# Kernel tuning notes

Measured on AMD Instinct MI355X. Metric: run time of the kernel, lower is better.

Reference implementation:

```python
import jax, jax.numpy as jnp
import numpy as np

DT = 0.2
N_VAR = 6
FEAT = 32


def _constants():
    dt = DT
    H = np.zeros((2, N_VAR), np.float32); H[0, 0] = 1.0; H[1, 3] = 1.0
    F = np.eye(N_VAR, dtype=np.float32)
    F[0, 1] = dt; F[0, 2] = dt * dt / 2; F[1, 2] = dt
    F[3, 4] = dt; F[3, 5] = dt * dt / 2; F[4, 5] = dt
    G = np.zeros((N_VAR, 2), np.float32)
    G[0, 0] = dt ** 3 / 6; G[1, 0] = dt * dt / 2; G[2, 0] = dt
    G[3, 1] = dt ** 3 / 6; G[4, 1] = dt * dt / 2; G[5, 1] = dt
    Bm = G.copy()  # B matrix equals G_ numerically
    return jnp.asarray(H), jnp.asarray(F), jnp.asarray(G), jnp.asarray(Bm)


def _inv2x2(S):
    a = S[..., 0, 0]; b = S[..., 0, 1]; c = S[..., 1, 0]; d = S[..., 1, 1]
    det = a * d - b * c
    inv = jnp.stack([jnp.stack([d, -b], -1), jnp.stack([-c, a], -1)], -2)
    return inv / det[..., None, None]


def _lstm(x, h, c, Wih, Whh, bih, bhh):
    gates = x @ Wih.T + bih + h @ Whh.T + bhh
    i, f, g, o = jnp.split(gates, 4, axis=-1)
    c2 = jax.nn.sigmoid(f) * c + jax.nn.sigmoid(i) * jnp.tanh(g)
    h2 = jax.nn.sigmoid(o) * jnp.tanh(c2)
    return h2, c2


def _forward(hist, position_std_x, position_std_y, velocity_std_x, velocity_std_y,
             acceleration_std_x, acceleration_std_y, jerk_std, coef_G, GR,
             cf_W, cf_b, lstm_Wih, lstm_Whh, lstm_bih, lstm_bhh, co_W, co_b, len_pred):
    H, F, G, Bm = _constants()
    Bsz = hist.shape[1]
    Z = hist[..., None]                          # (T, B, 2, 1)
    tanhG = jnp.tanh(coef_G)                     # (6,1)
    R = GR[:, None] * GR[None, :]                # (2,2)
    Gs_hist = G * tanhG * jerk_std               # (6,2)
    Q_hist = Gs_hist @ Gs_hist.T                 # (6,6)
    Id = jnp.eye(N_VAR, dtype=hist.dtype)

    # Kalman init
    V0 = (Z[1] - Z[0]) / DT                      # (B,2,1)
    X = jnp.einsum('ij,bjk->bik', H.T, Z[0])     # (B,6,1)
    X = X.at[:, 1, 0].set(V0[:, 0, 0]).at[:, 3, 0].set(V0[:, 1, 0])
    diagv = jnp.concatenate([position_std_x ** 2, velocity_std_x ** 2, acceleration_std_x ** 2,
                             position_std_y ** 2, velocity_std_y ** 2, acceleration_std_y ** 2])
    P = jnp.broadcast_to(jnp.diag(diagv), (Bsz, N_VAR, N_VAR)).astype(hist.dtype)
    h = jnp.zeros((Bsz, FEAT), hist.dtype)
    c = jnp.zeros((Bsz, FEAT), hist.dtype)

    def hist_step(carry, Zt):
        X, P, h, c = carry
        # LSTM state update (command output is discarded during history filtering)
        feat = jnp.tanh(X[:, :, 0] @ cf_W.T + cf_b)
        h, c = _lstm(feat, h, c, lstm_Wih, lstm_Whh, lstm_bih, lstm_bhh)
        # predict (no command)
        X = jnp.einsum('ij,bjk->bik', F, X)
        P = jnp.einsum('ij,bjk,lk->bil', F, P, F) + Q_hist
        # innovation
        y = Zt - jnp.einsum('ij,bjk->bik', H, X)
        S = jnp.einsum('ij,bjk,lk->bil', H, P, H) + R
        # update
        Sinv = _inv2x2(S)
        K = jnp.einsum('bij,kj,bkl->bil', P, H, Sinv)          # (B,6,2)
        X = X + K @ y
        ImKH = Id - jnp.einsum('bij,jk->bik', K, H)
        P = jnp.einsum('bij,bjk,blk->bil', ImKH, P, ImKH) + jnp.einsum('bij,jk,blk->bil', K, R, K)
        return (X, P, h, c), None

    (X, P, h, c), _ = jax.lax.scan(hist_step, (X, P, h, c), Z[1:])

    GtG = G * tanhG                                            # (6,2)

    def pred_step(carry, _):
        X, P, h, c = carry
        feat = jnp.tanh(X[:, :, 0] @ cf_W.T + cf_b)
        h, c = _lstm(feat, h, c, lstm_Wih, lstm_Whh, lstm_bih, lstm_bhh)
        command = h @ co_W.T + co_b                            # (B,4)
        X = jnp.einsum('ij,bjk->bik', F, X) + jnp.einsum('ij,bj->bi', Bm, command[:, :2])[:, :, None]
        Gs = jnp.einsum('ij,bj->bi', GtG, command[:, 2:])      # (B,6)
        Q = jnp.einsum('bi,bj->bij', Gs, Gs)
        P = jnp.einsum('ij,bjk,lk->bil', F, P, F) + Q
        mu = jnp.einsum('ij,bjk->bik', H, X)[:, :, 0]          # (B,2)
        Pout = jnp.einsum('ij,bjk,lk->bil', H, P, H)           # (B,2,2)
        return (X, P, h, c), (mu, Pout)

    _, (mu, Pout) = jax.lax.scan(pred_step, (X, P, h, c), None, length=len_pred)
    sx = jnp.sqrt(Pout[:, :, 0, 0])[..., None]
    sy = jnp.sqrt(Pout[:, :, 1, 1])[..., None]
    rho = (Pout[:, :, 0, 1] + Pout[:, :, 1, 0])[..., None] / (2 * sx * sy)
    return jnp.concatenate([mu, sx, sy, rho], axis=2)          # (len_pred, B, 5)


def setup_inputs() -> dict:
    key = jax.random.key(0)
    ks = jax.random.split(key, 8)
    T, B = 16, 32768
    u = lambda k, shape, fan: jax.random.uniform(k, shape, jnp.float32, -1.0, 1.0) / np.sqrt(fan)
    return {
        'hist': jax.random.normal(ks[0], (T, B, 2), jnp.float32),
        'position_std_x': jnp.ones((1,), jnp.float32) * 0.0519,
        'position_std_y': jnp.ones((1,), jnp.float32) * 1.7321,
        'velocity_std_x': jnp.ones((1,), jnp.float32) * 0.036,
        'velocity_std_y': jnp.ones((1,), jnp.float32) * 19.8837,
        'acceleration_std_x': jnp.ones((1,), jnp.float32) * 1e-05,
        'acceleration_std_y': jnp.ones((1,), jnp.float32) * 5.34,
        'jerk_std': jnp.array([[3.5043, 17.0283]], jnp.float32),
        'coef_G': jnp.array([[0.7427], [2.3545], [-0.0247], [-0.1391], [9.011], [0.0963]], jnp.float32),
        'GR': jnp.array([-0.0015, 0.001], jnp.float32),
        'cf_W': u(ks[1], (FEAT, N_VAR), N_VAR),
        'cf_b': u(ks[2], (FEAT,), N_VAR),
        'lstm_Wih': u(ks[3], (4 * FEAT, FEAT), FEAT),
        'lstm_Whh': u(ks[4], (4 * FEAT, FEAT), FEAT),
        'lstm_bih': u(ks[5], (4 * FEAT,), FEAT),
        'lstm_bhh': u(ks[6], (4 * FEAT,), FEAT),
        'co_W': u(ks[7], (4, FEAT), FEAT),
        'co_b': jnp.zeros((4,), jnp.float32),
        'len_pred': 25,
    }


def reference(hist, position_std_x, position_std_y, velocity_std_x, velocity_std_y,
              acceleration_std_x, acceleration_std_y, jerk_std, coef_G, GR,
              cf_W, cf_b, lstm_Wih, lstm_Whh, lstm_bih, lstm_bhh, co_W, co_b, len_pred):
    return _forward(hist, position_std_x, position_std_y, velocity_std_x, velocity_std_y,
                    acceleration_std_x, acceleration_std_y, jerk_std, coef_G, GR,
                    cf_W, cf_b, lstm_Wih, lstm_Whh, lstm_bih, lstm_bhh, co_W, co_b, int(len_pred))
```

## Files before the change

### kernel.cpp

```cpp
#include <hip/hip_runtime.h>
#include <hip/hip_bf16.h>
#include <math.h>

#define BLK 64
#define EPB 16
#define NF 32
#define THIST 15

typedef __attribute__((ext_vector_type(8))) short s16x8;
typedef __attribute__((ext_vector_type(4))) float f32x4;
typedef __attribute__((ext_vector_type(2))) float f32x2;

union frag_u { s16x8 v; unsigned u[4]; };

__device__ __forceinline__ float frcp(float x) {
    return __builtin_amdgcn_rcpf(x);
}
__device__ __forceinline__ float exp2b(float x) {
    return __builtin_amdgcn_exp2f(x);
}
__device__ __forceinline__ unsigned packbf2(float x0, float x1) {
    __hip_bfloat162 b = __float22bfloat162_rn(float2{x0, x1});
    union { __hip_bfloat162 b; unsigned u; } c; c.b = b; return c.u;
}
__device__ __forceinline__ float tanhfe(float x) {
    float e = __expf(2.0f * x);
    return fmaf(-2.0f, frcp(e + 1.0f), 1.0f);
}

__device__ __forceinline__ void fpft(float (&P)[6][6]) {
    const float dt = 0.2f, hd = 0.02f;
    #pragma unroll
    for (int j = 0; j < 6; ++j) {
        float a0 = P[0][j] + dt * P[1][j] + hd * P[2][j];
        float a1 = P[1][j] + dt * P[2][j];
        float a3 = P[3][j] + dt * P[4][j] + hd * P[5][j];
        float a4 = P[4][j] + dt * P[5][j];
        P[0][j] = a0; P[1][j] = a1; P[3][j] = a3; P[4][j] = a4;
    }
    #pragma unroll
    for (int i = 0; i < 6; ++i) {
        float a0 = P[i][0] + dt * P[i][1] + hd * P[i][2];
        float a1 = P[i][1] + dt * P[i][2];
        float a3 = P[i][3] + dt * P[i][4] + hd * P[i][5];
        float a4 = P[i][4] + dt * P[i][5];
        P[i][0] = a0; P[i][1] = a1; P[i][3] = a3; P[i][4] = a4;
    }
}

__global__ __launch_bounds__(BLK, 2)
void kalman_lstm(const float* __restrict__ hist,
                 const float* __restrict__ psx, const float* __restrict__ psy,
                 const float* __restrict__ vsx, const float* __restrict__ vsy,
                 const float* __restrict__ asx, const float* __restrict__ asy,
                 const float* __restrict__ jerk, const float* __restrict__ coefG,
                 const float* __restrict__ GRv,
                 const float* __restrict__ cfW, const float* __restrict__ cfb,
                 const float* __restrict__ Wih, const float* __restrict__ Whh,
                 const float* __restrict__ bih, const float* __restrict__ bhh,
                 const float* __restrict__ coW, const float* __restrict__ cob,
                 float* __restrict__ out, int B, int len_pred)
{
    __shared__ float kf[216];

    const int lane = threadIdx.x;
    const int e = lane & 15;
    const int s = lane >> 4;
    const int b = blockIdx.x * EPB + e;

    const float dt = 0.2f, hd = 0.02f;
    const float g0 = dt * dt * dt / 6.0f, g1 = 0.02f, g2 = dt;
    const float NL2E  = -1.4426950408889634f;
    const float T2L2E =  2.8853900817779268f;
    float ga0 = g0 * tanhf(coefG[0]);
    float ga1 = g1 * tanhf(coefG[1]);
    float ga2 = g2 * tanhf(coefG[2]);
    float gb3 = g0 * tanhf(coefG[3]);
    float gb4 = g1 * tanhf(coefG[4]);
    float gb5 = g2 * tanhf(coefG[5]);

    {
        float j0 = jerk[0], j1 = jerk[1];
        float gr0 = GRv[0], gr1 = GRv[1];
        float R00 = gr0 * gr0, R01 = gr0 * gr1, R11 = gr1 * gr1;
        float qa[3] = {ga0 * j0, ga1 * j0, ga2 * j0};
        float qb[3] = {gb3 * j1, gb4 * j1, gb5 * j1};

        float Pk[6][6];
        #pragma unroll
        for (int i = 0; i < 6; ++i)
            #pragma unroll
            for (int j = 0; j < 6; ++j) Pk[i][j] = 0.0f;
        { float v;
          v = psx[0]; Pk[0][0] = v * v;
          v = vsx[0]; Pk[1][1] = v * v;
          v = asx[0]; Pk[2][2] = v * v;
          v = psy[0]; Pk[3][3] = v * v;
          v = vsy[0]; Pk[4][4] = v * v;
          v = asy[0]; Pk[5][5] = v * v; }

        #pragma unroll 1
        for (int t = 0; t < THIST; ++t) {
            fpft(Pk);
            #pragma unroll
            for (int i = 0; i < 3; ++i)
                #pragma unroll
                for (int j = 0; j < 3; ++j) {
                    Pk[i][j]         += qa[i] * qa[j];
                    Pk[3 + i][3 + j] += qb[i] * qb[j];
                }
            float S00 = Pk[0][0] + R00;
            float S01 = Pk[0][3] + R01;
            float S11 = Pk[3][3] + R11;
            float idet = 1.0f / (S00 * S11 - S01 * S01);
            float i00 =  S11 * idet, i01 = -S01 * idet, i11 = S00 * idet;
            float K0[6], K1[6];
            #pragma unroll
            for (int i = 0; i < 6; ++i) {
                K0[i] = Pk[i][0] * i00 + Pk[i][3] * i01;
                K1[i] = Pk[i][0] * i01 + Pk[i][3] * i11;
            }
            if (lane == 0) {
                #pragma unroll
                for (int i = 0; i < 3; ++i) {
                    kf[t * 12 + 2 * i]     = K0[i];
                    kf[t * 12 + 2 * i + 1] = K0[3 + i];
                    kf[t * 12 + 6 + 2 * i]     = K1[i];
                    kf[t * 12 + 6 + 2 * i + 1] = K1[3 + i];
                }
            }
            #pragma unroll
            for (int i = 0; i < 6; ++i) {
                Pk[i][1] -= K0[1] * Pk[i][0] + K1[1] * Pk[i][3];
                Pk[i][2] -= K0[2] * Pk[i][0] + K1[2] * Pk[i][3];
                Pk[i][4] -= K0[4] * Pk[i][0] + K1[4] * Pk[i][3];
                Pk[i][5] -= K0[5] * Pk[i][0] + K1[5] * Pk[i][3];
                float t0 = Pk[i][0] - (K0[0] * Pk[i][0] + K1[0] * Pk[i][3]);
                float t3 = Pk[i][3] - (K0[3] * Pk[i][0] + K1[3] * Pk[i][3]);
                Pk[i][0] = t0; Pk[i][3] = t3;
            }
        }
        if (lane == 0) {
            #pragma unroll
            for (int i = 0; i < 6; ++i)
                #pragma unroll
                for (int j = 0; j < 6; ++j) kf[180 + i * 6 + j] = Pk[i][j];
        }
    }

    s16x8 wih_h[8], whh_h[8];
    #pragma unroll
    for (int nt = 0; nt < 8; ++nt) {
        int G = nt >> 1, blk = nt & 1;
        float sc = (G == 2) ? T2L2E : NL2E;
        int base = (G * 32 + 8 * (e >> 2) + 4 * blk + (e & 3)) * NF + s * 8;
        frag_u ih_h, hh_h;
        #pragma unroll
        for (int q = 0; q < 4; ++q) {
            ih_h.u[q] = packbf2(sc * Wih[base + 2 * q], sc * Wih[base + 2 * q + 1]);
            hh_h.u[q] = packbf2(sc * Whh[base + 2 * q], sc * Whh[base + 2 * q + 1]);
        }
        wih_h[nt] = ih_h.v;
        whh_h[nt] = hh_h.v;
    }

    f32x4 biasF[8];
    #pragma unroll
    for (int nt = 0; nt < 8; ++nt) {
        int G = nt >> 1, blk = nt & 1;
        float sc = (G == 2) ? T2L2E : NL2E;
        int base = G * 32 + 8 * s + 4 * blk;
        f32x4 bi = *(const f32x4*)&bih[base];
        f32x4 bh = *(const f32x4*)&bhh[base];
        biasF[nt] = (bi + bh) * sc;
    }

    s16x8 cfwA0, cfwA1;
    {
        frag_u fa0, fa1; fa0.v = (s16x8)0; fa1.v = (s16x8)0;
        if (s == 0) {
            int f0 = 8 * (e >> 2) + (e & 3);
            int f1 = f0 + 4;
            const float* w0 = cfW + f0 * 6;
            const float* w1 = cfW + f1 * 6;
            fa0.u[0] = packbf2(T2L2E * w0[0], T2L2E * w0[1]);
            fa0.u[1] = packbf2(T2L2E * w0[2], T2L2E * w0[3]);
            fa0.u[2] = packbf2(T2L2E * w0[4], T2L2E * w0[5]);
            fa0.u[3] = packbf2(T2L2E * cfb[f0], 0.0f);
            fa1.u[0] = packbf2(T2L2E * w1[0], T2L2E * w1[1]);
            fa1.u[1] = packbf2(T2L2E * w1[2], T2L2E * w1[3]);
            fa1.u[2] = packbf2(T2L2E * w1[4], T2L2E * w1[5]);
            fa1.u[3] = packbf2(T2L2E * cfb[f1], 0.0f);
        }
        cfwA0 = fa0.v; cfwA1 = fa1.v;
    }
    s16x8 cmdA;
    {
        frag_u ca;
        const float* cp = coW + (e & 3) * NF + 8 * s;
        #pragma unroll
        for (int q = 0; q < 4; ++q)
            ca.u[q] = packbf2(cp[2 * q], cp[2 * q + 1]);
        cmdA = ca.v;
    }
    f32x4 cobC = {cob[0], cob[1], cob[2], cob[3]};

    const float2* hist2 = (const float2*)hist;
    float2 z0 = hist2[b];
    float2 z1 = hist2[B + b];
    f32x2 Xa = {z0.x, (z1.y - z0.y) / dt};
    f32x2 Xb = {(z1.x - z0.x) / dt, 0.0f};
    f32x2 Xc = {0.0f, 0.0f};

    f32x2 creg2[4];
    #pragma unroll
    for (int j = 0; j < 4; ++j) creg2[j] = (f32x2){0.0f, 0.0f};
    s16x8 ah_h = (s16x8)0;

    __syncthreads();

    auto lstm_step = [&]() {
        frag_u xb;
        xb.u[0] = packbf2(Xa.x, Xb.x);
        xb.u[1] = packbf2(Xc.x, Xa.y);
        xb.u[2] = packbf2(Xb.y, Xc.y);
        xb.u[3] = 0x00003f80u;
        const f32x4 zc4 = {0.0f, 0.0f, 0.0f, 0.0f};
        f32x4 fp0 = __builtin_amdgcn_mfma_f32_16x16x32_bf16(cfwA0, xb.v, zc4, 0, 0, 0);
        f32x4 fp1 = __builtin_amdgcn_mfma_f32_16x16x32_bf16(cfwA1, xb.v, zc4, 0, 0, 0);
        auto tanh2p = [](float x0, float x1) -> f32x2 {
            f32x2 eg2 = {exp2b(x0), exp2b(x1)};
            f32x2 gp  = eg2 + 1.0f;
            f32x2 rd  = {frcp(gp.x), frcp(gp.y)};
            return (f32x2){1.0f, 1.0f} - 2.0f * rd;
        };
        frag_u af;
        { f32x2 t = tanh2p(fp0[0], fp0[1]); af.u[0] = packbf2(t.x, t.y); }
        { f32x2 t = tanh2p(fp0[2], fp0[3]); af.u[1] = packbf2(t.x, t.y); }
        { f32x2 t = tanh2p(fp1[0], fp1[1]); af.u[2] = packbf2(t.x, t.y); }
        { f32x2 t = tanh2p(fp1[2], fp1[3]); af.u[3] = packbf2(t.x, t.y); }

        f32x4 acc[8];
        #pragma unroll
        for (int nt = 0; nt < 8; ++nt) {
            acc[nt] = __builtin_amdgcn_mfma_f32_16x16x32_bf16(wih_h[nt], af.v, biasF[nt], 0, 0, 0);
            acc[nt] = __builtin_amdgcn_mfma_f32_16x16x32_bf16(whh_h[nt], ah_h, acc[nt], 0, 0, 0);
        }

        unsigned whx[2][2];
        #pragma unroll
        for (int blk = 0; blk < 2; ++blk) {
            #pragma unroll
            for (int rp = 0; rp < 2; ++rp) {
                int r0 = 2 * rp, r1 = 2 * rp + 1;
                f32x2 ei2 = {exp2b(acc[0 + blk][r0]), exp2b(acc[0 + blk][r1])};
                f32x2 ef2 = {exp2b(acc[2 + blk][r0]), exp2b(acc[2 + blk][r1])};
                f32x2 eg2 = {exp2b(acc[4 + blk][r0]), exp2b(acc[4 + blk][r1])};
                f32x2 eo2 = {exp2b(acc[6 + blk][r0]), exp2b(acc[6 + blk][r1])};
                f32x2 a2  = ef2 + 1.0f;
                f32x2 b2  = (ei2 + 1.0f) * (eg2 + 1.0f);
                f32x2 num = (eg2 - 1.0f) * a2 + creg2[2 * blk + rp] * b2;
                f32x2 den = a2 * b2;
                f32x2 rd  = {frcp(den.x), frcp(den.y)};
                f32x2 cn2 = num * rd;
                creg2[2 * blk + rp] = cn2;
                f32x2 cns = T2L2E * cn2;
                f32x2 ec2 = {exp2b(cns.x), exp2b(cns.y)};
                f32x2 d2  = (eo2 + 1.0f) * (ec2 + 1.0f);
                f32x2 rd2 = {frcp(d2.x), frcp(d2.y)};
                f32x2 hv2 = (ec2 - 1.0f) * rd2;
                whx[blk][rp] = packbf2(hv2.x, hv2.y);
            }
        }

        frag_u ahh;
        ahh.u[0] = whx[0][0];
        ahh.u[1] = whx[0][1];
        ahh.u[2] = whx[1][0];
        ahh.u[3] = whx[1][1];
        ah_h = ahh.v;
    };

    float2 zc = z1;
    #pragma unroll 1
    for (int t = 0; t < THIST; ++t) {
        int tn = (t + 2 < 16) ? (t + 2) : 15;
        float2 zn = hist2[(size_t)tn * B + b];
        f32x4 k0 = *(const f32x4*)&kf[t * 12];
        f32x4 k1 = *(const f32x4*)&kf[t * 12 + 4];
        f32x4 k2 = *(const f32x4*)&kf[t * 12 + 8];

        lstm_step();

        Xa = Xa + dt * Xb + hd * Xc;
        Xb = Xb + dt * Xc;
        float y0 = zc.x - Xa.x, y1 = zc.y - Xa.y;
        f32x2 kA0 = {k0[0], k0[1]}, kB0 = {k0[2], k0[3]}, kC0 = {k1[0], k1[1]};
        f32x2 kA1 = {k1[2], k1[3]}, kB1 = {k2[0], k2[1]}, kC1 = {k2[2], k2[3]};
        Xa = Xa + kA0 * y0 + kA1 * y1;
        Xb = Xb + kB0 * y0 + kB1 * y1;
        Xc = Xc + kC0 * y0 + kC1 * y1;
        zc = zn;
    }

    f32x2 pxy00 = {kf[180], kf[201]}, pxy01 = {kf[181], kf[202]},
          pxy02 = {kf[182], kf[203]}, pxy11 = {kf[187], kf[208]},
          pxy12 = {kf[188], kf[209]}, pxy22 = {kf[194], kf[214]};
    float c00 = kf[183], c01 = kf[184], c02 = kf[185],
          c10 = kf[189], c11 = kf[190], c12 = kf[191],
          c20 = kf[195], c21 = kf[196], c22 = kf[197];
    const f32x2 gaP0 = {ga0, gb3}, gaP1 = {ga1, gb4}, gaP2 = {ga2, gb5};

    #pragma unroll 1
    for (int tp = 0; tp < len_pred; ++tp) {
        lstm_step();

        f32x4 cm = __builtin_amdgcn_mfma_f32_16x16x32_bf16(cmdA, ah_h, cobC, 0, 0, 0);
        f32x2 cmdP  = {cm[0], cm[1]};
        f32x2 cmd23 = {cm[2], cm[3]};

        Xa = Xa + dt * Xb + hd * Xc + g0 * cmdP;
        Xb = Xb + dt * Xc + g1 * cmdP;
        Xc = Xc + g2 * cmdP;

        f32x2 gsA = gaP0 * cmd23;
        f32x2 gsB = gaP1 * cmd23;
        f32x2 gsC = gaP2 * cmd23;
        {
            f32x2 r00 = pxy00 + dt * pxy01 + hd * pxy02;
            f32x2 r01 = pxy01 + dt * pxy11 + hd * pxy12;
            f32x2 r02 = pxy02 + dt * pxy12 + hd * pxy22;
            f32x2 r11 = pxy11 + dt * pxy12;
            f32x2 r12 = pxy12 + dt * pxy22;
            pxy00 = r00 + dt * r01 + hd * r02;
            pxy01 = r01 + dt * r02;
            pxy02 = r02;
            pxy11 = r11 + dt * r12;
            pxy12 = r12;
            pxy00 += gsA * gsA; pxy01 += gsA * gsB; pxy02 += gsA * gsC;
            pxy11 += gsB * gsB; pxy12 += gsB * gsC; pxy22 += gsC * gsC;
        }
        {
            float gs0 = gsA.x, gs1 = gsB.x, gs2 = gsC.x;
            float gs3 = gsA.y, gs4 = gsB.y, gs5 = gsC.y;
            float q00 = c00 + dt * c10 + hd * c20;
            float q01 = c01 + dt * c11 + hd * c21;
            float q02 = c02 + dt * c12 + hd * c22;
            float q10 = c10 + dt * c20;
            float q11 = c11 + dt * c21;
            float q12 = c12 + dt * c22;
            c00 = q00 + dt * q01 + hd * q02;
            c01 = q01 + dt * q02;
            c02 = q02;
            c10 = q10 + dt * q11 + hd * q12;
            c11 = q11 + dt * q12;
            c12 = q12;
            float n20 = c20 + dt * c21 + hd * c22;
            float n21 = c21 + dt * c22;
            c20 = n20; c21 = n21;
            c00 += gs0 * gs3; c01 += gs0 * gs4; c02 += gs0 * gs5;
            c10 += gs1 * gs3; c11 += gs1 * gs4; c12 += gs1 * gs5;
            c20 += gs2 * gs3; c21 += gs2 * gs4; c22 += gs2 * gs5;
        }

        float sx = sqrtf(pxy00.x), sy = sqrtf(pxy00.y);
        float rho = c00 / (sx * sy);
        if (s == 0) {
            size_t o = ((size_t)tp * B + b) * 5u;
            out[o + 0] = Xa.x;
            out[o + 1] = Xa.y;
            out[o + 2] = sx;
            out[o + 3] = sy;
            out[o + 4] = rho;
        }
    }
}

extern "C" void kernel_launch(void* const* d_in, const int* in_sizes, int n_in,
                              void* d_out, int out_size, void* d_ws, size_t ws_size,
                              hipStream_t stream) {
    const int T = 16;
    const int B = in_sizes[0] / (2 * T);
    const int len_pred = out_size / (5 * B);
    (void)d_ws; (void)ws_size; (void)n_in;

    const int grid = (B + EPB - 1) / EPB;
    kalman_lstm<<<grid, BLK, 0, stream>>>(
        (const float*)d_in[0],  (const float*)d_in[1],  (const float*)d_in[2],
        (const float*)d_in[3],  (const float*)d_in[4],  (const float*)d_in[5],
        (const float*)d_in[6],  (const float*)d_in[7],  (const float*)d_in[8],
        (const float*)d_in[9],  (const float*)d_in[10], (const float*)d_in[11],
        (const float*)d_in[12], (const float*)d_in[13], (const float*)d_in[14],
        (const float*)d_in[15], (const float*)d_in[16], (const float*)d_in[17],
        (float*)d_out, B, len_pred);
}
```

Measured before the change: 173.3 us.

## Software-pipeline LSTM feature computation and covariance update across timesteps

Splits the LSTM step into a feature stage (coordinate MFMA plus tanh) and a core gate stage. The feature input for the next step is computed right after the Kalman state update, and in the prediction loop the covariance update and output store are delayed by one iteration so they can overlap with the next LSTM core's MFMA latency. This targets the serial dependency chain per step, at the cost of more live registers and a peeled prologue and epilogue.

```diff
diff --git a/kernel.cpp b/kernel.cpp
--- a/kernel.cpp
+++ b/kernel.cpp
@@ -216,10 +216,11 @@
     #pragma unroll
     for (int j = 0; j < 4; ++j) creg2[j] = (f32x2){0.0f, 0.0f};
     s16x8 ah_h = (s16x8)0;
+    frag_u af_c;
 
     __syncthreads();
 
-    auto lstm_step = [&]() {
+    auto compute_feat = [&]() {
         frag_u xb;
         xb.u[0] = packbf2(Xa.x, Xb.x);
         xb.u[1] = packbf2(Xc.x, Xa.y);
@@ -234,16 +235,17 @@
             f32x2 rd  = {frcp(gp.x), frcp(gp.y)};
             return (f32x2){1.0f, 1.0f} - 2.0f * rd;
         };
-        frag_u af;
-        { f32x2 t = tanh2p(fp0[0], fp0[1]); af.u[0] = packbf2(t.x, t.y); }
-        { f32x2 t = tanh2p(fp0[2], fp0[3]); af.u[1] = packbf2(t.x, t.y); }
-        { f32x2 t = tanh2p(fp1[0], fp1[1]); af.u[2] = packbf2(t.x, t.y); }
-        { f32x2 t = tanh2p(fp1[2], fp1[3]); af.u[3] = packbf2(t.x, t.y); }
-
+        { f32x2 t = tanh2p(fp0[0], fp0[1]); af_c.u[0] = packbf2(t.x, t.y); }
+        { f32x2 t = tanh2p(fp0[2], fp0[3]); af_c.u[1] = packbf2(t.x, t.y); }
+        { f32x2 t = tanh2p(fp1[0], fp1[1]); af_c.u[2] = packbf2(t.x, t.y); }
+        { f32x2 t = tanh2p(fp1[2], fp1[3]); af_c.u[3] = packbf2(t.x, t.y); }
+    };
+
+    auto lstm_core = [&]() {
         f32x4 acc[8];
         #pragma unroll
         for (int nt = 0; nt < 8; ++nt) {
-            acc[nt] = __builtin_amdgcn_mfma_f32_16x16x32_bf16(wih_h[nt], af.v, biasF[nt], 0, 0, 0);
+            acc[nt] = __builtin_amdgcn_mfma_f32_16x16x32_bf16(wih_h[nt], af_c.v, biasF[nt], 0, 0, 0);
             acc[nt] = __builtin_amdgcn_mfma_f32_16x16x32_bf16(whh_h[nt], ah_h, acc[nt], 0, 0, 0);
         }
 
@@ -281,6 +283,7 @@
         ah_h = ahh.v;
     };
 
+    compute_feat();
     float2 zc = z1;
     #pragma unroll 1
     for (int t = 0; t < THIST; ++t) {
@@ -290,7 +293,7 @@
         f32x4 k1 = *(const f32x4*)&kf[t * 12 + 4];
         f32x4 k2 = *(const f32x4*)&kf[t * 12 + 8];
 
-        lstm_step();
+        lstm_core();
 
         Xa = Xa + dt * Xb + hd * Xc;
         Xb = Xb + dt * Xc;
@@ -301,6 +304,7 @@
         Xb = Xb + kB0 * y0 + kB1 * y1;
         Xc = Xc + kC0 * y0 + kC1 * y1;
         zc = zn;
+        compute_feat();
     }
 
     f32x2 pxy00 = {kf[180], kf[201]}, pxy01 = {kf[181], kf[202]},
@@ -311,18 +315,7 @@
           c20 = kf[195], c21 = kf[196], c22 = kf[197];
     const f32x2 gaP0 = {ga0, gb3}, gaP1 = {ga1, gb4}, gaP2 = {ga2, gb5};
 
-    #pragma unroll 1
-    for (int tp = 0; tp < len_pred; ++tp) {
-        lstm_step();
-
-        f32x4 cm = __builtin_amdgcn_mfma_f32_16x16x32_bf16(cmdA, ah_h, cobC, 0, 0, 0);
-        f32x2 cmdP  = {cm[0], cm[1]};
-        f32x2 cmd23 = {cm[2], cm[3]};
-
-        Xa = Xa + dt * Xb + hd * Xc + g0 * cmdP;
-        Xb = Xb + dt * Xc + g1 * cmdP;
-        Xc = Xc + g2 * cmdP;
-
+    auto pupdate = [&](f32x2 cmd23) {
         f32x2 gsA = gaP0 * cmd23;
         f32x2 gsB = gaP1 * cmd23;
         f32x2 gsC = gaP2 * cmd23;
@@ -362,13 +355,56 @@
             c10 += gs1 * gs3; c11 += gs1 * gs4; c12 += gs1 * gs5;
             c20 += gs2 * gs3; c21 += gs2 * gs4; c22 += gs2 * gs5;
         }
-
+    };
+
+    lstm_core();
+    f32x4 cm = __builtin_amdgcn_mfma_f32_16x16x32_bf16(cmdA, ah_h, cobC, 0, 0, 0);
+    {
+        f32x2 cmdP = {cm[0], cm[1]};
+        Xa = Xa + dt * Xb + hd * Xc + g0 * cmdP;
+        Xb = Xb + dt * Xc + g1 * cmdP;
+        Xc = Xc + g2 * cmdP;
+    }
+    f32x2 XoutSv = Xa;
+    f32x2 cmdSv  = {cm[2], cm[3]};
+    compute_feat();
+
+    #pragma unroll 1
+    for (int tp = 1; tp < len_pred; ++tp) {
+        lstm_core();
+
+        pupdate(cmdSv);
+        {
+            float sx = sqrtf(pxy00.x), sy = sqrtf(pxy00.y);
+            float rho = c00 / (sx * sy);
+            if (s == 0) {
+                size_t o = ((size_t)(tp - 1) * B + b) * 5u;
+                out[o + 0] = XoutSv.x;
+                out[o + 1] = XoutSv.y;
+                out[o + 2] = sx;
+                out[o + 3] = sy;
+                out[o + 4] = rho;
+            }
+        }
+
+        cm = __builtin_amdgcn_mfma_f32_16x16x32_bf16(cmdA, ah_h, cobC, 0, 0, 0);
+        f32x2 cmdP = {cm[0], cm[1]};
+        Xa = Xa + dt * Xb + hd * Xc + g0 * cmdP;
+        Xb = Xb + dt * Xc + g1 * cmdP;
+        Xc = Xc + g2 * cmdP;
+        XoutSv = Xa;
+        cmdSv  = (f32x2){cm[2], cm[3]};
+        if (tp < len_pred - 1) compute_feat();
+    }
+
+    pupdate(cmdSv);
+    {
         float sx = sqrtf(pxy00.x), sy = sqrtf(pxy00.y);
         float rho = c00 / (sx * sy);
         if (s == 0) {
-            size_t o = ((size_t)tp * B + b) * 5u;
-            out[o + 0] = Xa.x;
-            out[o + 1] = Xa.y;
+            size_t o = ((size_t)(len_pred - 1) * B + b) * 5u;
+            out[o + 0] = XoutSv.x;
+            out[o + 1] = XoutSv.y;
             out[o + 2] = sx;
             out[o + 3] = sy;
             out[o + 4] = rho;
```

Measured after the change: 175.6 us. About the same (+1.3%).
